# Kernel tuning notes

Measured on AMD Instinct MI355X. Metric: run time of the kernel, lower is better.

The kernel has to match this reference:

```python
import jax, jax.numpy as jnp
import numpy as np

N = 4096        # sequence length
H = 16          # heads
D_MODEL = 1024
D_HEAD = D_MODEL // H  # 64


def setup_inputs() -> dict:
    key = jax.random.key(0)
    ks = jax.random.split(key, 9)
    scale = 1.0 / np.sqrt(D_MODEL)
    inp = {
        "X_Q": jax.random.normal(ks[0], (N, D_MODEL), dtype=jnp.float32),
        "X_K": jax.random.normal(ks[1], (N, D_MODEL), dtype=jnp.float32),
        "X_V": jax.random.normal(ks[2], (N, D_MODEL), dtype=jnp.float32),
        # per-head projection weights, stacked over head axis: [H, D_MODEL, D_HEAD]
        "Wq": jax.random.normal(ks[3], (H, D_MODEL, D_HEAD), dtype=jnp.float32) * scale,
        "bq": jax.random.normal(ks[4], (H, D_HEAD), dtype=jnp.float32) * scale,
        "Wk": jax.random.normal(ks[5], (H, D_MODEL, D_HEAD), dtype=jnp.float32) * scale,
        "bk": jax.random.normal(ks[6], (H, D_HEAD), dtype=jnp.float32) * scale,
        "Wv": jax.random.normal(ks[7], (H, D_MODEL, D_HEAD), dtype=jnp.float32) * scale,
        "bv": jax.random.normal(ks[8], (H, D_HEAD), dtype=jnp.float32) * scale,
    }
    return inp


def reference(X_Q, X_K, X_V, Wq, bq, Wk, bk, Wv, bv):
    # Batched per-head projections (replaces the Python loop of nn.Linear calls)
    Q = jnp.einsum("nd,hdk->hnk", X_Q, Wq) + bq[:, None, :]   # [H, N, D_HEAD]
    K = jnp.einsum("nd,hdk->hnk", X_K, Wk) + bk[:, None, :]
    V = jnp.einsum("nd,hdk->hnk", X_V, Wv) + bv[:, None, :]
    scores = jnp.einsum("hnk,hmk->hnm", Q, K) / jnp.sqrt(jnp.float32(D_HEAD))  # [H, N, N]
    attn = jax.nn.softmax(scores, axis=-1)  # softmax over keys (dim=1 of the [n,n] per-head matrix)
    out = jnp.einsum("hnm,hmv->hnv", attn, V)  # [H, N, D_HEAD]
    # concat heads along feature dim -> [N, D_MODEL]
    return jnp.transpose(out, (1, 0, 2)).reshape(N, D_MODEL)
```

## Files before the change

kernel.cpp:

```cpp
#include <hip/hip_runtime.h>

typedef unsigned short u16;
typedef __attribute__((ext_vector_type(8))) short bf16x8;
typedef __attribute__((ext_vector_type(16))) float floatx16;

#define C2 0.18033688011112042f
#define TRUNC_BIAS 0.99859f

static __device__ __forceinline__ u16 f2b(float f) {
  unsigned u = __builtin_bit_cast(unsigned, f);
  u = (u + 0x7FFFu + ((u >> 16) & 1u)) >> 16;
  return (u16)u;
}
static __device__ __forceinline__ unsigned pk2(float a, float b) {
  return (unsigned)f2b(a) | ((unsigned)f2b(b) << 16);
}
static __device__ __forceinline__ void gl_lds16(const void* g, void* l) {
  __builtin_amdgcn_global_load_lds(
      (const __attribute__((address_space(1))) unsigned*)g,
      (__attribute__((address_space(3))) unsigned*)l, 16, 0, 0);
}
static __device__ __forceinline__ float ex2(float x) {
#if __has_builtin(__builtin_amdgcn_exp2f)
  return __builtin_amdgcn_exp2f(x);
#else
  return exp2f(x);
#endif
}
static __device__ __forceinline__ unsigned pkt(float a, float b) {
#if __has_builtin(__builtin_amdgcn_perm)
  return __builtin_amdgcn_perm(__builtin_bit_cast(unsigned, a),
                               __builtin_bit_cast(unsigned, b), 0x03020706u);
#else
  return (__builtin_bit_cast(unsigned, a) >> 16) |
         (__builtin_bit_cast(unsigned, b) & 0xffff0000u);
#endif
}
static __device__ __forceinline__ void pswap(unsigned& a, unsigned& b) {
#if __has_builtin(__builtin_amdgcn_permlane32_swap)
  auto r = __builtin_amdgcn_permlane32_swap(a, b, false, false);
  a = r[0];
  b = r[1];
#else
  unsigned ta = (unsigned)__shfl_xor((int)a, 32);
  unsigned tb = (unsigned)__shfl_xor((int)b, 32);
  bool hi = (threadIdx.x & 32) != 0;
  unsigned na = hi ? tb : a;
  unsigned nb = hi ? b : ta;
  a = na;
  b = nb;
#endif
}

__global__ __launch_bounds__(256) void conv_k(
    const float* __restrict__ x0, const float* __restrict__ x1, const float* __restrict__ x2,
    u16* __restrict__ o0, u16* __restrict__ o1, u16* __restrict__ o2,
    const float* __restrict__ w0, const float* __restrict__ w1, const float* __restrict__ w2,
    u16* __restrict__ t0, u16* __restrict__ t1, u16* __restrict__ t2) {
  __shared__ __align__(16) float tile[64 * 68];
  int bx = blockIdx.x, t = threadIdx.x;
  if (bx < 6144) {
    int z = bx >> 11;
    const float* x = z == 0 ? x0 : (z == 1 ? x1 : x2);
    u16* o = z == 0 ? o0 : (z == 1 ? o1 : o2);
    size_t i = (((size_t)(bx & 2047)) * 256 + t) * 8;
    float4 a = *(const float4*)(x + i);
    float4 b = *(const float4*)(x + i + 4);
    uint4 u;
    u.x = pk2(a.x, a.y); u.y = pk2(a.z, a.w);
    u.z = pk2(b.x, b.y); u.w = pk2(b.z, b.w);
    *(uint4*)(o + i) = u;
  } else {
    int idx = bx - 6144;
    int z = idx >> 8, b = idx & 255;
    const float* W = z == 0 ? w0 : (z == 1 ? w1 : w2);
    u16* O = z == 0 ? t0 : (z == 1 ? t1 : t2);
    const float s = (z == 0) ? C2 : 1.0f;
    int h = b >> 4, d0 = (b & 15) * 64;
    {
      int r = t >> 2, c = t & 3;
      const float* src = W + (size_t)h * 65536 + (size_t)(d0 + r) * 64 + c * 16;
#pragma unroll
      for (int i = 0; i < 4; ++i) {
        float4 v = *(const float4*)(src + 4 * i);
        *(float4*)&tile[r * 68 + c * 16 + 4 * i] = v;
      }
    }
    __syncthreads();
    {
      int k = t >> 2, dc = t & 3;
      unsigned u[8];
#pragma unroll
      for (int i = 0; i < 8; ++i) {
        float a = tile[(dc * 16 + 2 * i) * 68 + k] * s;
        float bb = tile[(dc * 16 + 2 * i + 1) * 68 + k] * s;
        u[i] = pk2(a, bb);
      }
      u16* dst = O + ((size_t)(h * 64 + k)) * 1024 + d0 + dc * 16;
      *(uint4*)dst = make_uint4(u[0], u[1], u[2], u[3]);
      *(uint4*)(dst + 8) = make_uint4(u[4], u[5], u[6], u[7]);
    }
  }
}

__global__ __launch_bounds__(256, 3) void proj_k(
    const u16* __restrict__ x0, const u16* __restrict__ x1, const u16* __restrict__ x2,
    const u16* __restrict__ w0, const u16* __restrict__ w1, const u16* __restrict__ w2,
    const float* __restrict__ b0, const float* __restrict__ b1, const float* __restrict__ b2,
    u16* __restrict__ p0, u16* __restrict__ p1, u16* __restrict__ p2) {
  int z = blockIdx.z;
  const u16* X = z == 0 ? x0 : (z == 1 ? x1 : x2);
  const u16* Wt = z == 0 ? w0 : (z == 1 ? w1 : w2);
  const float* bias = z == 0 ? b0 : (z == 1 ? b1 : b2);
  u16* outP = z == 0 ? p0 : (z == 1 ? p1 : p2);
  const float bsc = (z == 0) ? C2 : 1.0f;

  __shared__ uint4 smem4[16384 / 16];
  char* sm = (char*)smem4;
  const int t = threadIdx.x, lane = t & 63, wid = t >> 6;
  const int L = lane & 31, h2 = lane >> 5;
  const int wm = wid >> 1, wc = wid & 1;
  const int rowt = blockIdx.x + 8 * (blockIdx.y & 3);
  const int colt = blockIdx.y >> 2;
  const int n0 = rowt * 128, c0 = colt * 128;

  floatx16 acc[2][2];
  if (z <= 1) {
    const float* bp = bias + c0 + wc * 64;
#pragma unroll
    for (int ci = 0; ci < 2; ++ci)
#pragma unroll
      for (int r = 0; r < 16; ++r) {
        int rr = (r & 3) + 8 * (r >> 2) + 4 * h2;
        float bv = bp[ci * 32 + rr] * bsc;
        acc[ci][0][r] = bv;
        acc[ci][1][r] = bv;
      }
  } else {
#pragma unroll
    for (int ct = 0; ct < 2; ++ct) {
      float bv = bias[c0 + wc * 64 + ct * 32 + L];
#pragma unroll
      for (int mt = 0; mt < 2; ++mt)
#pragma unroll
        for (int r = 0; r < 16; ++r) acc[mt][ct][r] = bv;
    }
  }

  const int srow = t >> 2, sc = t & 3;
  for (int k0 = 0; k0 < 1024; k0 += 32) {
#pragma unroll
    for (int i = 0; i < 2; ++i) {
      int row = i * 64 + srow;
      int cg = sc ^ ((row >> 1) & 3);
      gl_lds16(X + (size_t)(n0 + row) * 1024 + k0 + cg * 8, sm + i * 4096 + wid * 1024);
    }
#pragma unroll
    for (int i = 0; i < 2; ++i) {
      int row = i * 64 + srow;
      int cg = sc ^ ((row >> 1) & 3);
      gl_lds16(Wt + (size_t)(c0 + row) * 1024 + k0 + cg * 8, sm + 8192 + i * 4096 + wid * 1024);
    }
    __syncthreads();
#pragma unroll
    for (int ks = 0; ks < 2; ++ks) {
      bf16x8 af[2], bfr[2];
#pragma unroll
      for (int mt = 0; mt < 2; ++mt) {
        int m = wm * 64 + mt * 32 + L;
        int cc = (2 * ks + h2) ^ ((m >> 1) & 3);
        af[mt] = *(const bf16x8*)(sm + m * 64 + cc * 16);
      }
#pragma unroll
      for (int ct = 0; ct < 2; ++ct) {
        int c = wc * 64 + ct * 32 + L;
        int cc = (2 * ks + h2) ^ ((c >> 1) & 3);
        bfr[ct] = *(const bf16x8*)(sm + 8192 + c * 64 + cc * 16);
      }
      if (z <= 1) {
#pragma unroll
        for (int ci = 0; ci < 2; ++ci)
#pragma unroll
          for (int ni = 0; ni < 2; ++ni)
            acc[ci][ni] = __builtin_amdgcn_mfma_f32_32x32x16_bf16(bfr[ci], af[ni], acc[ci][ni], 0, 0, 0);
      } else {
#pragma unroll
        for (int mt = 0; mt < 2; ++mt)
#pragma unroll
          for (int ct = 0; ct < 2; ++ct)
            acc[mt][ct] = __builtin_amdgcn_mfma_f32_32x32x16_bf16(af[mt], bfr[ct], acc[mt][ct], 0, 0, 0);
      }
    }
    __syncthreads();
  }

  const int hh = (c0 >> 6) + wc;
#pragma unroll
  for (int a0 = 0; a0 < 2; ++a0)
#pragma unroll
    for (int a1 = 0; a1 < 2; ++a1) {
      unsigned pk[8];
#pragma unroll
      for (int g = 0; g < 8; ++g) pk[g] = pk2(acc[a0][a1][2 * g], acc[a0][a1][2 * g + 1]);
      pswap(pk[0], pk[2]);
      pswap(pk[1], pk[3]);
      pswap(pk[4], pk[6]);
      pswap(pk[5], pk[7]);
#pragma unroll
      for (int q2 = 0; q2 < 2; ++q2) {
        uint4 u = make_uint4(pk[q2 * 4], pk[q2 * 4 + 1], pk[q2 * 4 + 2], pk[q2 * 4 + 3]);
        size_t slot;
        if (z <= 1) {
          int T = (n0 + wm * 64 + a1 * 32) >> 5;
          int ks = a0 * 2 + q2;
          slot = (size_t)hh * 32768 + (size_t)(T * 4 + ks) * 64 + lane;
        } else {
          int T = (n0 + wm * 64 + a0 * 32) >> 5;
          slot = (size_t)hh * 32768 + (size_t)(T * 4 + a1 * 2 + q2) * 64 + lane;
        }
        *(uint4*)(outP + (slot << 3)) = u;
      }
    }
}

__global__ __launch_bounds__(512, 2) void attn_k(
    const u16* __restrict__ Qp, const u16* __restrict__ Kp, const u16* __restrict__ Vp,
    float* __restrict__ out) {
  __shared__ __align__(16) float Ob[2][64 * 68];
  __shared__ float lstat[8][64];
  const int t = threadIdx.x, lane = t & 63, w = t >> 6;
  const int L = lane & 31, h2 = lane >> 5;
  const int ws = w & 1, kh = w >> 1;
  const int h = blockIdx.x & 15, qb = blockIdx.x >> 4;
  const int n0 = qb * 128 + ws * 64;
  const u16* Qph = Qp + (size_t)h * 262144;
  const u16* Kph = Kp + (size_t)h * 262144;
  const u16* Vph = Vp + (size_t)h * 262144;
  const int tbase = kh * 32;

  bf16x8 qf[2][4];
#pragma unroll
  for (int nt = 0; nt < 2; ++nt) {
    int Tq = qb * 4 + ws * 2 + nt;
#pragma unroll
    for (int ks = 0; ks < 4; ++ks)
      qf[nt][ks] = *(const bf16x8*)(Qph + (((size_t)(Tq * 4 + ks)) << 9) + lane * 8);
  }

  const floatx16 FZ = {0.f, 0.f, 0.f, 0.f, 0.f, 0.f, 0.f, 0.f,
                       0.f, 0.f, 0.f, 0.f, 0.f, 0.f, 0.f, 0.f};
  floatx16 accO[2][2];
#pragma unroll
  for (int a = 0; a < 2; ++a)
#pragma unroll
    for (int b = 0; b < 2; ++b) accO[a][b] = FZ;
  float l_run[2] = {0.f, 0.f};

  bf16x8 kfA[4], kfB[4], vfA[4], vfB[4];
  auto loadK = [&](int rn, bf16x8* kf) {
    const u16* p = Kph + ((size_t)(tbase + rn) << 11) + lane * 8;
#pragma unroll
    for (int ks = 0; ks < 4; ++ks) kf[ks] = *(const bf16x8*)(p + ks * 512);
  };
  auto loadV = [&](int rn, bf16x8* vf) {
    const u16* p = Vph + ((size_t)(tbase + rn) << 11) + lane * 8;
#pragma unroll
    for (int idx = 0; idx < 4; ++idx) vf[idx] = *(const bf16x8*)(p + idx * 512);
  };
  loadK(0, kfA);
  loadV(0, vfA);

  auto round = [&](int r, bf16x8* kf, bf16x8* vf, bf16x8* kfn, bf16x8* vfn) {
    floatx16 accS[2];
    accS[0] = __builtin_amdgcn_mfma_f32_32x32x16_bf16(kf[0], qf[0][0], FZ, 0, 0, 0);
    accS[1] = __builtin_amdgcn_mfma_f32_32x32x16_bf16(kf[0], qf[1][0], FZ, 0, 0, 0);
#pragma unroll
    for (int ks = 1; ks < 4; ++ks) {
      accS[0] = __builtin_amdgcn_mfma_f32_32x32x16_bf16(kf[ks], qf[0][ks], accS[0], 0, 0, 0);
      accS[1] = __builtin_amdgcn_mfma_f32_32x32x16_bf16(kf[ks], qf[1][ks], accS[1], 0, 0, 0);
    }
    int rn = (r + 1) & 31;
    loadK(rn, kfn);
    loadV(rn, vfn);

    unsigned pkr[2][8];
#pragma unroll
    for (int nt = 0; nt < 2; ++nt) {
      float p[16];
      float s0 = 0.f, s1 = 0.f;
#pragma unroll
      for (int q = 0; q < 16; q += 2) {
        p[q] = ex2(accS[nt][q]);
        p[q + 1] = ex2(accS[nt][q + 1]);
        s0 += p[q];
        s1 += p[q + 1];
      }
      l_run[nt] += s0 + s1;
#pragma unroll
      for (int g = 0; g < 8; ++g) pkr[nt][g] = pkt(p[2 * g], p[2 * g + 1]);
      pswap(pkr[nt][0], pkr[nt][2]);
      pswap(pkr[nt][1], pkr[nt][3]);
      pswap(pkr[nt][4], pkr[nt][6]);
      pswap(pkr[nt][5], pkr[nt][7]);
    }

#pragma unroll
    for (int c2 = 0; c2 < 2; ++c2) {
      bf16x8 pf[2];
#pragma unroll
      for (int nt = 0; nt < 2; ++nt) {
        uint4 u = make_uint4(pkr[nt][c2 * 4], pkr[nt][c2 * 4 + 1],
                             pkr[nt][c2 * 4 + 2], pkr[nt][c2 * 4 + 3]);
        pf[nt] = __builtin_bit_cast(bf16x8, u);
      }
#pragma unroll
      for (int vt = 0; vt < 2; ++vt) {
        accO[vt][0] = __builtin_amdgcn_mfma_f32_32x32x16_bf16(vf[vt * 2 + c2], pf[0], accO[vt][0], 0, 0, 0);
        accO[vt][1] = __builtin_amdgcn_mfma_f32_32x32x16_bf16(vf[vt * 2 + c2], pf[1], accO[vt][1], 0, 0, 0);
      }
    }
  };

  for (int r = 0; r < 32; r += 2) {
    round(r, kfA, vfA, kfB, vfB);
    round(r + 1, kfB, vfB, kfA, vfA);
  }

  l_run[0] += __shfl_xor(l_run[0], 32);
  l_run[1] += __shfl_xor(l_run[1], 32);
  if (h2 == 0) {
    lstat[w][L] = l_run[0];
    lstat[w][32 + L] = l_run[1];
  }
  if (kh == 1) {
#pragma unroll
    for (int vt = 0; vt < 2; ++vt)
#pragma unroll
      for (int nt = 0; nt < 2; ++nt)
#pragma unroll
        for (int g = 0; g < 4; ++g)
          *(float4*)&Ob[ws][(nt * 32 + L) * 68 + vt * 32 + 8 * g + 4 * h2] =
              make_float4(accO[vt][nt][4 * g], accO[vt][nt][4 * g + 1],
                          accO[vt][nt][4 * g + 2], accO[vt][nt][4 * g + 3]);
  }
  __syncthreads();
  if (kh == 2) {
#pragma unroll
    for (int vt = 0; vt < 2; ++vt)
#pragma unroll
      for (int nt = 0; nt < 2; ++nt)
#pragma unroll
        for (int g = 0; g < 4; ++g) {
          float* q = &Ob[ws][(nt * 32 + L) * 68 + vt * 32 + 8 * g + 4 * h2];
          float4 o = *(const float4*)q;
          o.x += accO[vt][nt][4 * g];
          o.y += accO[vt][nt][4 * g + 1];
          o.z += accO[vt][nt][4 * g + 2];
          o.w += accO[vt][nt][4 * g + 3];
          *(float4*)q = o;
        }
  }
  __syncthreads();
  if (kh == 3) {
#pragma unroll
    for (int vt = 0; vt < 2; ++vt)
#pragma unroll
      for (int nt = 0; nt < 2; ++nt)
#pragma unroll
        for (int g = 0; g < 4; ++g) {
          float* q = &Ob[ws][(nt * 32 + L) * 68 + vt * 32 + 8 * g + 4 * h2];
          float4 o = *(const float4*)q;
          o.x += accO[vt][nt][4 * g];
          o.y += accO[vt][nt][4 * g + 1];
          o.z += accO[vt][nt][4 * g + 2];
          o.w += accO[vt][nt][4 * g + 3];
          *(float4*)q = o;
        }
  }
  __syncthreads();
  if (kh == 0) {
    float scale[2];
#pragma unroll
    for (int nt = 0; nt < 2; ++nt) {
      int idx = nt * 32 + L;
      float lt = lstat[ws][idx] + lstat[2 + ws][idx] + lstat[4 + ws][idx] + lstat[6 + ws][idx];
      scale[nt] = 1.f / (lt * TRUNC_BIAS);
    }
#pragma unroll
    for (int vt = 0; vt < 2; ++vt)
#pragma unroll
      for (int nt = 0; nt < 2; ++nt)
#pragma unroll
        for (int g = 0; g < 4; ++g) {
          float4 o = *(const float4*)&Ob[ws][(nt * 32 + L) * 68 + vt * 32 + 8 * g + 4 * h2];
          float4 res;
          res.x = (accO[vt][nt][4 * g] + o.x) * scale[nt];
          res.y = (accO[vt][nt][4 * g + 1] + o.y) * scale[nt];
          res.z = (accO[vt][nt][4 * g + 2] + o.z) * scale[nt];
          res.w = (accO[vt][nt][4 * g + 3] + o.w) * scale[nt];
          *(float4*)(out + ((size_t)(n0 + nt * 32 + L)) * 1024 + h * 64 + vt * 32 + 8 * g + 4 * h2) = res;
        }
  }
}

extern "C" void kernel_launch(void* const* d_in, const int* in_sizes, int n_in,
                              void* d_out, int out_size, void* d_ws, size_t ws_size,
                              hipStream_t stream) {
  const float* XQ = (const float*)d_in[0];
  const float* XK = (const float*)d_in[1];
  const float* XV = (const float*)d_in[2];
  const float* Wq = (const float*)d_in[3];
  const float* bq = (const float*)d_in[4];
  const float* Wk = (const float*)d_in[5];
  const float* bk = (const float*)d_in[6];
  const float* Wv = (const float*)d_in[7];
  const float* bv = (const float*)d_in[8];

  const size_t MB = 1024 * 1024;
  char* w = (char*)d_ws;
  u16* xqb = (u16*)(w + 0 * MB);
  u16* xkb = (u16*)(w + 8 * MB);
  u16* xvb = (u16*)(w + 16 * MB);
  u16* wtq = (u16*)(w + 24 * MB);
  u16* wtk = (u16*)(w + 26 * MB);
  u16* wtv = (u16*)(w + 28 * MB);
  u16* Qpk = (u16*)(w + 32 * MB);
  u16* Kpk = (u16*)(w + 40 * MB);
  u16* Vpk = (u16*)(w + 48 * MB);

  conv_k<<<dim3(6912), 256, 0, stream>>>(XQ, XK, XV, xqb, xkb, xvb,
                                         Wq, Wk, Wv, wtq, wtk, wtv);
  proj_k<<<dim3(8, 32, 3), 256, 0, stream>>>(xqb, xkb, xvb, wtq, wtk, wtv,
                                             bq, bk, bv, Qpk, Kpk, Vpk);
  attn_k<<<dim3(512), 512, 0, stream>>>(Qpk, Kpk, Vpk, (float*)d_out);
}
```

Baseline: 236.7 us.

## Software-pipeline QK^T with softmax/PV in attention, widen query tile, deepen proj K-step

The attention kernel now uses 4 query warps and 2 key-split warps per block, so each block covers 256 queries and the grid is half as large. It also software-pipelines the next tile's QK^T MFMAs against the current tile's exp and PV MFMAs, and cuts the cross-warp reduction to a single LDS stage. The projection kernel doubles its K-step per LDS stage to 64 and uses an 8-way XOR swizzle, which halves barrier count but doubles shared memory. Keeping extra S accumulators live raises register pressure, and 256 blocks may underfill the 256 CUs at 2 blocks per CU.

```diff
diff --git a/kernel.cpp b/kernel.cpp
--- a/kernel.cpp
+++ b/kernel.cpp
@@ -115,7 +115,7 @@
   u16* outP = z == 0 ? p0 : (z == 1 ? p1 : p2);
   const float bsc = (z == 0) ? C2 : 1.0f;
 
-  __shared__ uint4 smem4[16384 / 16];
+  __shared__ uint4 smem4[32768 / 16];
   char* sm = (char*)smem4;
   const int t = threadIdx.x, lane = t & 63, wid = t >> 6;
   const int L = lane & 31, h2 = lane >> 5;
@@ -147,35 +147,35 @@
     }
   }
 
-  const int srow = t >> 2, sc = t & 3;
-  for (int k0 = 0; k0 < 1024; k0 += 32) {
-#pragma unroll
-    for (int i = 0; i < 2; ++i) {
-      int row = i * 64 + srow;
-      int cg = sc ^ ((row >> 1) & 3);
+  const int srow = t >> 3, sc = t & 7;
+  for (int k0 = 0; k0 < 1024; k0 += 64) {
+#pragma unroll
+    for (int i = 0; i < 4; ++i) {
+      int row = i * 32 + srow;
+      int cg = sc ^ (row & 7);
       gl_lds16(X + (size_t)(n0 + row) * 1024 + k0 + cg * 8, sm + i * 4096 + wid * 1024);
     }
 #pragma unroll
-    for (int i = 0; i < 2; ++i) {
-      int row = i * 64 + srow;
-      int cg = sc ^ ((row >> 1) & 3);
-      gl_lds16(Wt + (size_t)(c0 + row) * 1024 + k0 + cg * 8, sm + 8192 + i * 4096 + wid * 1024);
+    for (int i = 0; i < 4; ++i) {
+      int row = i * 32 + srow;
+      int cg = sc ^ (row & 7);
+      gl_lds16(Wt + (size_t)(c0 + row) * 1024 + k0 + cg * 8, sm + 16384 + i * 4096 + wid * 1024);
     }
     __syncthreads();
 #pragma unroll
-    for (int ks = 0; ks < 2; ++ks) {
+    for (int ks = 0; ks < 4; ++ks) {
       bf16x8 af[2], bfr[2];
 #pragma unroll
       for (int mt = 0; mt < 2; ++mt) {
         int m = wm * 64 + mt * 32 + L;
-        int cc = (2 * ks + h2) ^ ((m >> 1) & 3);
-        af[mt] = *(const bf16x8*)(sm + m * 64 + cc * 16);
+        int cc = (ks * 2 + h2) ^ (m & 7);
+        af[mt] = *(const bf16x8*)(sm + m * 128 + cc * 16);
       }
 #pragma unroll
       for (int ct = 0; ct < 2; ++ct) {
         int c = wc * 64 + ct * 32 + L;
-        int cc = (2 * ks + h2) ^ ((c >> 1) & 3);
-        bfr[ct] = *(const bf16x8*)(sm + 8192 + c * 64 + cc * 16);
+        int cc = (ks * 2 + h2) ^ (c & 7);
+        bfr[ct] = *(const bf16x8*)(sm + 16384 + c * 128 + cc * 16);
       }
       if (z <= 1) {
 #pragma unroll
@@ -226,22 +226,22 @@
 __global__ __launch_bounds__(512, 2) void attn_k(
     const u16* __restrict__ Qp, const u16* __restrict__ Kp, const u16* __restrict__ Vp,
     float* __restrict__ out) {
-  __shared__ __align__(16) float Ob[2][64 * 68];
+  __shared__ __align__(16) float Ob[4][64 * 68];
   __shared__ float lstat[8][64];
   const int t = threadIdx.x, lane = t & 63, w = t >> 6;
   const int L = lane & 31, h2 = lane >> 5;
-  const int ws = w & 1, kh = w >> 1;
-  const int h = blockIdx.x & 15, qb = blockIdx.x >> 4;
-  const int n0 = qb * 128 + ws * 64;
+  const int ws = w & 3, kh = w >> 2;
+  const int h = blockIdx.x & 15, qt = blockIdx.x >> 4;
+  const int n0 = qt * 256 + ws * 64;
   const u16* Qph = Qp + (size_t)h * 262144;
   const u16* Kph = Kp + (size_t)h * 262144;
   const u16* Vph = Vp + (size_t)h * 262144;
-  const int tbase = kh * 32;
+  const int tbase = kh * 64;
 
   bf16x8 qf[2][4];
 #pragma unroll
   for (int nt = 0; nt < 2; ++nt) {
-    int Tq = qb * 4 + ws * 2 + nt;
+    int Tq = qt * 8 + ws * 2 + nt;
 #pragma unroll
     for (int ks = 0; ks < 4; ++ks)
       qf[nt][ks] = *(const bf16x8*)(Qph + (((size_t)(Tq * 4 + ks)) << 9) + lane * 8);
@@ -267,63 +267,60 @@
 #pragma unroll
     for (int idx = 0; idx < 4; ++idx) vf[idx] = *(const bf16x8*)(p + idx * 512);
   };
+
+  floatx16 Scur[2], Snxt[2];
+  auto halfround = [&](floatx16& Sc, floatx16& Sn, const bf16x8* kfn, const bf16x8* vfc, int nt) {
+    Sn = __builtin_amdgcn_mfma_f32_32x32x16_bf16(kfn[0], qf[nt][0], FZ, 0, 0, 0);
+#pragma unroll
+    for (int ks = 1; ks < 4; ++ks)
+      Sn = __builtin_amdgcn_mfma_f32_32x32x16_bf16(kfn[ks], qf[nt][ks], Sn, 0, 0, 0);
+    float p[16];
+    float s0 = 0.f, s1 = 0.f;
+#pragma unroll
+    for (int q = 0; q < 16; q += 2) {
+      p[q] = ex2(Sc[q]);
+      p[q + 1] = ex2(Sc[q + 1]);
+      s0 += p[q];
+      s1 += p[q + 1];
+    }
+    l_run[nt] += s0 + s1;
+    unsigned pk[8];
+#pragma unroll
+    for (int g = 0; g < 8; ++g) pk[g] = pkt(p[2 * g], p[2 * g + 1]);
+    pswap(pk[0], pk[2]);
+    pswap(pk[1], pk[3]);
+    pswap(pk[4], pk[6]);
+    pswap(pk[5], pk[7]);
+#pragma unroll
+    for (int c2 = 0; c2 < 2; ++c2) {
+      uint4 u = make_uint4(pk[c2 * 4], pk[c2 * 4 + 1], pk[c2 * 4 + 2], pk[c2 * 4 + 3]);
+      bf16x8 pf = __builtin_bit_cast(bf16x8, u);
+      accO[0][nt] = __builtin_amdgcn_mfma_f32_32x32x16_bf16(vfc[c2], pf, accO[0][nt], 0, 0, 0);
+      accO[1][nt] = __builtin_amdgcn_mfma_f32_32x32x16_bf16(vfc[2 + c2], pf, accO[1][nt], 0, 0, 0);
+    }
+  };
+
   loadK(0, kfA);
   loadV(0, vfA);
-
-  auto round = [&](int r, bf16x8* kf, bf16x8* vf, bf16x8* kfn, bf16x8* vfn) {
-    floatx16 accS[2];
-    accS[0] = __builtin_amdgcn_mfma_f32_32x32x16_bf16(kf[0], qf[0][0], FZ, 0, 0, 0);
-    accS[1] = __builtin_amdgcn_mfma_f32_32x32x16_bf16(kf[0], qf[1][0], FZ, 0, 0, 0);
-#pragma unroll
-    for (int ks = 1; ks < 4; ++ks) {
-      accS[0] = __builtin_amdgcn_mfma_f32_32x32x16_bf16(kf[ks], qf[0][ks], accS[0], 0, 0, 0);
-      accS[1] = __builtin_amdgcn_mfma_f32_32x32x16_bf16(kf[ks], qf[1][ks], accS[1], 0, 0, 0);
-    }
-    int rn = (r + 1) & 31;
-    loadK(rn, kfn);
-    loadV(rn, vfn);
-
-    unsigned pkr[2][8];
-#pragma unroll
-    for (int nt = 0; nt < 2; ++nt) {
-      float p[16];
-      float s0 = 0.f, s1 = 0.f;
-#pragma unroll
-      for (int q = 0; q < 16; q += 2) {
-        p[q] = ex2(accS[nt][q]);
-        p[q + 1] = ex2(accS[nt][q + 1]);
-        s0 += p[q];
-        s1 += p[q + 1];
-      }
-      l_run[nt] += s0 + s1;
-#pragma unroll
-      for (int g = 0; g < 8; ++g) pkr[nt][g] = pkt(p[2 * g], p[2 * g + 1]);
-      pswap(pkr[nt][0], pkr[nt][2]);
-      pswap(pkr[nt][1], pkr[nt][3]);
-      pswap(pkr[nt][4], pkr[nt][6]);
-      pswap(pkr[nt][5], pkr[nt][7]);
-    }
-
-#pragma unroll
-    for (int c2 = 0; c2 < 2; ++c2) {
-      bf16x8 pf[2];
-#pragma unroll
-      for (int nt = 0; nt < 2; ++nt) {
-        uint4 u = make_uint4(pkr[nt][c2 * 4], pkr[nt][c2 * 4 + 1],
-                             pkr[nt][c2 * 4 + 2], pkr[nt][c2 * 4 + 3]);
-        pf[nt] = __builtin_bit_cast(bf16x8, u);
-      }
-#pragma unroll
-      for (int vt = 0; vt < 2; ++vt) {
-        accO[vt][0] = __builtin_amdgcn_mfma_f32_32x32x16_bf16(vf[vt * 2 + c2], pf[0], accO[vt][0], 0, 0, 0);
-        accO[vt][1] = __builtin_amdgcn_mfma_f32_32x32x16_bf16(vf[vt * 2 + c2], pf[1], accO[vt][1], 0, 0, 0);
-      }
-    }
-  };
-
-  for (int r = 0; r < 32; r += 2) {
-    round(r, kfA, vfA, kfB, vfB);
-    round(r + 1, kfB, vfB, kfA, vfA);
+  Scur[0] = __builtin_amdgcn_mfma_f32_32x32x16_bf16(kfA[0], qf[0][0], FZ, 0, 0, 0);
+  Scur[1] = __builtin_amdgcn_mfma_f32_32x32x16_bf16(kfA[0], qf[1][0], FZ, 0, 0, 0);
+#pragma unroll
+  for (int ks = 1; ks < 4; ++ks) {
+    Scur[0] = __builtin_amdgcn_mfma_f32_32x32x16_bf16(kfA[ks], qf[0][ks], Scur[0], 0, 0, 0);
+    Scur[1] = __builtin_amdgcn_mfma_f32_32x32x16_bf16(kfA[ks], qf[1][ks], Scur[1], 0, 0, 0);
+  }
+  loadK(1, kfB);
+  loadV(1, vfB);
+
+  for (int r = 0; r < 64; r += 2) {
+    loadK((r + 2) & 63, kfA);
+    halfround(Scur[0], Snxt[0], kfB, vfA, 0);
+    halfround(Scur[1], Snxt[1], kfB, vfA, 1);
+    loadV((r + 2) & 63, vfA);
+    loadK((r + 3) & 63, kfB);
+    halfround(Snxt[0], Scur[0], kfA, vfB, 0);
+    halfround(Snxt[1], Scur[1], kfA, vfB, 1);
+    loadV((r + 3) & 63, vfB);
   }
 
   l_run[0] += __shfl_xor(l_run[0], 32);
@@ -344,48 +341,11 @@
                           accO[vt][nt][4 * g + 2], accO[vt][nt][4 * g + 3]);
   }
   __syncthreads();
-  if (kh == 2) {
-#pragma unroll
-    for (int vt = 0; vt < 2; ++vt)
-#pragma unroll
-      for (int nt = 0; nt < 2; ++nt)
-#pragma unroll
-        for (int g = 0; g < 4; ++g) {
-          float* q = &Ob[ws][(nt * 32 + L) * 68 + vt * 32 + 8 * g + 4 * h2];
-          float4 o = *(const float4*)q;
-          o.x += accO[vt][nt][4 * g];
-          o.y += accO[vt][nt][4 * g + 1];
-          o.z += accO[vt][nt][4 * g + 2];
-          o.w += accO[vt][nt][4 * g + 3];
-          *(float4*)q = o;
-        }
-  }
-  __syncthreads();
-  if (kh == 3) {
-#pragma unroll
-    for (int vt = 0; vt < 2; ++vt)
-#pragma unroll
-      for (int nt = 0; nt < 2; ++nt)
-#pragma unroll
-        for (int g = 0; g < 4; ++g) {
-          float* q = &Ob[ws][(nt * 32 + L) * 68 + vt * 32 + 8 * g + 4 * h2];
-          float4 o = *(const float4*)q;
-          o.x += accO[vt][nt][4 * g];
-          o.y += accO[vt][nt][4 * g + 1];
-          o.z += accO[vt][nt][4 * g + 2];
-          o.w += accO[vt][nt][4 * g + 3];
-          *(float4*)q = o;
-        }
-  }
-  __syncthreads();
   if (kh == 0) {
     float scale[2];
 #pragma unroll
-    for (int nt = 0; nt < 2; ++nt) {
-      int idx = nt * 32 + L;
-      float lt = lstat[ws][idx] + lstat[2 + ws][idx] + lstat[4 + ws][idx] + lstat[6 + ws][idx];
-      scale[nt] = 1.f / (lt * TRUNC_BIAS);
-    }
+    for (int nt = 0; nt < 2; ++nt)
+      scale[nt] = 1.f / ((lstat[w][nt * 32 + L] + lstat[w + 4][nt * 32 + L]) * TRUNC_BIAS);
 #pragma unroll
     for (int vt = 0; vt < 2; ++vt)
 #pragma unroll
@@ -432,5 +392,5 @@
                                          Wq, Wk, Wv, wtq, wtk, wtv);
   proj_k<<<dim3(8, 32, 3), 256, 0, stream>>>(xqb, xkb, xvb, wtq, wtk, wtv,
                                              bq, bk, bv, Qpk, Kpk, Vpk);
-  attn_k<<<dim3(512), 512, 0, stream>>>(Qpk, Kpk, Vpk, (float*)d_out);
-}
+  attn_k<<<dim3(256), 512, 0, stream>>>(Qpk, Kpk, Vpk, (float*)d_out);
+}
```

Result: faster. 225.3 us (-4.8%).
